# Performance work log

Measured on AMD Instinct MI355X. Metric: run time of the kernel, lower is better.

The kernel has to match this reference:

```python
import jax, jax.numpy as jnp
import numpy as np

D_MODEL = 1024
NUM_HEADS = 16
HEAD_DIM = D_MODEL // NUM_HEADS
ROPE_BASE = 10000.0


def _rotate_half(x):
    x1, x2 = jnp.split(x, 2, axis=-1)
    return jnp.concatenate([-x2, x1], axis=-1)


def _rope_cache(seq_len, head_dim, dtype):
    half = head_dim // 2
    inv_freq = 1.0 / (ROPE_BASE ** (jnp.arange(half, dtype=jnp.float32) / float(half)))
    t = jnp.arange(seq_len, dtype=jnp.float32)
    freqs = t[:, None] * inv_freq[None, :]          # [s, half]
    emb = jnp.concatenate([freqs, freqs], axis=-1)   # [s, head_dim]
    cos = jnp.cos(emb)[None, None, :, :].astype(dtype)  # [1,1,s,d]
    sin = jnp.sin(emb)[None, None, :, :].astype(dtype)
    return cos, sin


def setup_inputs() -> dict:
    key = jax.random.key(0)
    k1, k2, k3 = jax.random.split(key, 3)
    b, s = 4, 2048
    x = jax.random.normal(k1, (b, s, D_MODEL), dtype=jnp.float32)
    mask = jnp.ones((b, s), dtype=jnp.float32)
    Wqkv = jax.random.normal(k2, (D_MODEL, 3 * D_MODEL), dtype=jnp.float32) * (D_MODEL ** -0.5)
    Wout = jax.random.normal(k3, (D_MODEL, D_MODEL), dtype=jnp.float32) * (D_MODEL ** -0.5)
    return {"x": x, "mask": mask, "Wqkv": Wqkv, "Wout": Wout}


def reference(x, mask, Wqkv, Wout):
    b, s, _ = x.shape
    qkv = x @ Wqkv                                   # [b,s,3*d_model]
    q, k, v = jnp.split(qkv, 3, axis=-1)

    def split_heads(t):
        return t.reshape(b, s, NUM_HEADS, HEAD_DIM).transpose(0, 2, 1, 3)  # [b,h,s,d]

    q, k, v = map(split_heads, (q, k, v))
    cos, sin = _rope_cache(s, HEAD_DIM, x.dtype)
    q = q * cos + _rotate_half(q) * sin
    k = k * cos + _rotate_half(k) * sin

    scale = HEAD_DIM ** -0.5
    logits = jnp.einsum('bhid,bhjd->bhij', q, k) * scale
    logits = logits + (1.0 - mask)[:, None, None, :] * -1e9
    attn = jax.nn.softmax(logits, axis=-1)
    out = jnp.einsum('bhij,bhjd->bhid', attn, v)     # [b,h,s,d]
    out = out.transpose(0, 2, 1, 3).reshape(b, s, D_MODEL)
    return out @ Wout
```

## Files before the change

### kernel.cpp

```cpp
#include <hip/hip_runtime.h>

typedef unsigned short u16;
typedef unsigned int u32;
typedef int i32x2 __attribute__((ext_vector_type(2)));
typedef float f32x4 __attribute__((ext_vector_type(4)));
typedef float f32x16 __attribute__((ext_vector_type(16)));
typedef __bf16 bf16x8 __attribute__((ext_vector_type(8)));
typedef unsigned short u16x8 __attribute__((ext_vector_type(8)));
typedef unsigned short u16x4 __attribute__((ext_vector_type(4)));
typedef unsigned int u32x4 __attribute__((ext_vector_type(4)));

#define S_ 2048
#define DM 1024

#define LDS_U32(p) ((__attribute__((address_space(3))) unsigned int*)(p))
#define GLB_U32(p) ((const __attribute__((address_space(1))) unsigned int*)(p))

__device__ __forceinline__ u16 f2bf(float f) {
    unsigned int u = __float_as_uint(f);
    u += 0x7fffu + ((u >> 16) & 1u);
    return (u16)(u >> 16);
}
__device__ __forceinline__ float bf2f(u16 s) {
    return __uint_as_float(((unsigned int)s) << 16);
}
__device__ __forceinline__ float fast_exp2(float x) {
#if __has_builtin(__builtin_amdgcn_exp2f)
    return __builtin_amdgcn_exp2f(x);
#else
    return __expf(x * 0.69314718056f);
#endif
}

__global__ __launch_bounds__(256) void f32_to_bf16_kernel(const float* __restrict__ in,
                                                          u16* __restrict__ o, int n) {
    int i = (blockIdx.x * 256 + threadIdx.x) << 2;
    if (i >= n) return;
    float4 f = *(const float4*)&in[i];
    u16x4 r;
    r[0] = f2bf(f.x); r[1] = f2bf(f.y); r[2] = f2bf(f.z); r[3] = f2bf(f.w);
    *(u16x4*)&o[i] = r;
}

__global__ __launch_bounds__(256) void transpose_w(const float* __restrict__ W,
                                                   u16* __restrict__ Wt, int K, int N) {
    __shared__ float tile[32][33];
    int nb = blockIdx.x << 5, kb = blockIdx.y << 5;
    int tx = threadIdx.x & 31, ty = threadIdx.x >> 5;
#pragma unroll
    for (int r = 0; r < 32; r += 8)
        tile[ty + r][tx] = W[(size_t)(kb + ty + r) * N + nb + tx];
    __syncthreads();
#pragma unroll
    for (int r = 0; r < 32; r += 8)
        Wt[(size_t)(nb + ty + r) * K + kb + tx] = f2bf(tile[tx][ty + r]);
}

template <int MODE>
__global__ __launch_bounds__(256) void gemm_bt(const u16* __restrict__ A,
                                               const u16* __restrict__ Bt,
                                               float* __restrict__ Cf,
                                               u16* __restrict__ Qp, u16* __restrict__ Kp,
                                               u16* __restrict__ Vp,
                                               int M, int N, int K) {
    __shared__ __align__(16) u16 Al[128 * 32];
    __shared__ __align__(16) u16 Bl[128 * 32];
    const int tid = threadIdx.x;
    const int Ntiles = N >> 7;
    const int cpx = gridDim.x >> 3;
    const int bid = (int)blockIdx.x;
    const int wg = (bid & 7) * cpx + (bid >> 3);
    const int mt = wg / Ntiles, nt = wg % Ntiles;
    const int m0 = mt << 7, n0 = nt << 7;
    const int wave = tid >> 6, lane = tid & 63;
    const int wm = (wave >> 1) << 6, wn = (wave & 1) << 6;
    const int lr = lane & 15, lk = (lane >> 4) << 3;

    const int srow = (wave << 4) + (lane >> 2);
    const int scol = (lane & 3) << 3;

    f32x4 acc[4][4] = {};

    for (int k0 = 0; k0 < K; k0 += 32) {
        __syncthreads();
#pragma unroll
        for (int i = 0; i < 2; ++i) {
            const u16* ga = &A[(size_t)(m0 + srow + (i << 6)) * K + k0 + scol];
            const u16* gb = &Bt[(size_t)(n0 + srow + (i << 6)) * K + k0 + scol];
            __builtin_amdgcn_global_load_lds(GLB_U32(ga), LDS_U32(&Al[(wave << 9) + (i << 11)]), 16, 0, 0);
            __builtin_amdgcn_global_load_lds(GLB_U32(gb), LDS_U32(&Bl[(wave << 9) + (i << 11)]), 16, 0, 0);
        }
        __syncthreads();
        bf16x8 af[4], bfr[4];
#pragma unroll
        for (int i = 0; i < 4; ++i) {
            af[i]  = __builtin_bit_cast(bf16x8, *(const u16x8*)&Al[(wm + (i << 4) + lr) * 32 + lk]);
            bfr[i] = __builtin_bit_cast(bf16x8, *(const u16x8*)&Bl[(wn + (i << 4) + lr) * 32 + lk]);
        }
#pragma unroll
        for (int i = 0; i < 4; ++i)
#pragma unroll
            for (int j = 0; j < 4; ++j)
                acc[i][j] = __builtin_amdgcn_mfma_f32_16x16x32_bf16(af[i], bfr[j], acc[i][j], 0, 0, 0);
    }

    if (MODE == 0) {
        const int t = (n0 + wn) >> 10;
        if (t < 2) {
            const float LN1E4_32 = 9.210340371976184f / 32.0f;
            const float invf0 = __expf(-(float)lr * LN1E4_32);
            const float invf1 = __expf(-(float)(lr + 16) * LN1E4_32);
#pragma unroll
            for (int i = 0; i < 4; ++i) {
                const int rbase = m0 + wm + (i << 4) + ((lane >> 4) << 2);
#pragma unroll
                for (int jj = 0; jj < 4; ++jj) {
                    const float s = (float)((rbase + jj) & (S_ - 1));
                    float sn0, c0, sn1, c1;
                    __sincosf(s * invf0, &sn0, &c0);
                    __sincosf(s * invf1, &sn1, &c1);
                    const float v0 = acc[i][0][jj], v1 = acc[i][1][jj];
                    const float v2 = acc[i][2][jj], v3 = acc[i][3][jj];
                    acc[i][0][jj] = v0 * c0 - v2 * sn0;
                    acc[i][2][jj] = v2 * c0 + v0 * sn0;
                    acc[i][1][jj] = v1 * c1 - v3 * sn1;
                    acc[i][3][jj] = v3 * c1 + v1 * sn1;
                }
            }
        }
    }

#pragma unroll
    for (int i = 0; i < 4; ++i) {
#pragma unroll
        for (int j = 0; j < 4; ++j) {
            int rbase = m0 + wm + (i << 4) + ((lane >> 4) << 2);
            int col = n0 + wn + (j << 4) + lr;
#pragma unroll
            for (int jj = 0; jj < 4; ++jj) {
                float val = acc[i][j][jj];
                int row = rbase + jj;
                if (MODE == 0) {
                    int t = col >> 10, rem = col & 1023;
                    int h = rem >> 6, d = rem & 63;
                    int b = row >> 11, s = row & 2047;
                    size_t dst = ((size_t)((b << 4) + h) * S_ + s) * 64 + d;
                    u16 bv = f2bf(val);
                    if (t == 0) Qp[dst] = bv;
                    else if (t == 1) Kp[dst] = bv;
                    else Vp[dst] = bv;
                } else {
                    Cf[(size_t)row * N + col] = val;
                }
            }
        }
    }
}

__global__ __launch_bounds__(256) void vtrans_kernel(const u16* __restrict__ v,
                                                     u16* __restrict__ vt) {
    __shared__ __align__(16) u16 t[64][72];
    const int bh = blockIdx.x >> 5, st = blockIdx.x & 31;
    const size_t base = (size_t)bh * (S_ * 64);
    const int s0 = st << 6;
    const int r = threadIdx.x >> 2, c0 = (threadIdx.x & 3) << 4;
    *(u16x8*)&t[r][c0]     = *(const u16x8*)&v[base + (size_t)(s0 + r) * 64 + c0];
    *(u16x8*)&t[r][c0 + 8] = *(const u16x8*)&v[base + (size_t)(s0 + r) * 64 + c0 + 8];
    __syncthreads();
    u16x8 w0, w1;
#pragma unroll
    for (int i = 0; i < 8; ++i) w0[i] = t[c0 + i][r];
#pragma unroll
    for (int i = 0; i < 8; ++i) w1[i] = t[c0 + 8 + i][r];
    *(u16x8*)&vt[base + (size_t)r * S_ + s0 + c0]     = w0;
    *(u16x8*)&vt[base + (size_t)r * S_ + s0 + c0 + 8] = w1;
}

__device__ __forceinline__ void softmax_chain(f32x16* p, f32x16* acc,
                                              float& m_run, float& l_run,
                                              u32* wa, u32* wb,
                                              const float* madd_tile, bool hasmask,
                                              float* bcast_w, int c, int hi) {
    if (hasmask) {
#pragma unroll
        for (int tt = 0; tt < 2; ++tt)
#pragma unroll
            for (int rq = 0; rq < 4; ++rq) {
                float4 mf = *(const float4*)&madd_tile[tt * 32 + rq * 8 + hi * 4];
                p[tt][4 * rq + 0] += mf.x;
                p[tt][4 * rq + 1] += mf.y;
                p[tt][4 * rq + 2] += mf.z;
                p[tt][4 * rq + 3] += mf.w;
            }
    }

    float tm[16];
#pragma unroll
    for (int r = 0; r < 16; ++r) tm[r] = fmaxf(p[0][r], p[1][r]);
    float a0 = fmaxf(fmaxf(tm[0], tm[1]), tm[2]);
    float a1 = fmaxf(fmaxf(tm[3], tm[4]), tm[5]);
    float a2 = fmaxf(fmaxf(tm[6], tm[7]), tm[8]);
    float a3 = fmaxf(fmaxf(tm[9], tm[10]), tm[11]);
    float a4 = fmaxf(fmaxf(tm[12], tm[13]), tm[14]);
    float b0 = fmaxf(fmaxf(a0, a1), a2);
    float b1 = fmaxf(fmaxf(a3, a4), tm[15]);
    float mx = fmaxf(b0, b1);
    {
        i32x2 mm = __builtin_amdgcn_permlane32_swap(__float_as_int(mx), __float_as_int(mx), false, false);
        mx = fmaxf(__int_as_float(mm[0]), __int_as_float(mm[1]));
    }

    if (!__all(mx - m_run <= 8.0f)) {
        float mnew = fmaxf(m_run, mx);
        float alpha = fast_exp2(m_run - mnew);
        m_run = mnew;
        l_run *= alpha;
        bcast_w[c] = alpha;
        float avf[16];
#pragma unroll
        for (int rq = 0; rq < 4; ++rq) {
            float4 t4 = *(const float4*)&bcast_w[rq * 8 + hi * 4];
            avf[4 * rq + 0] = t4.x; avf[4 * rq + 1] = t4.y;
            avf[4 * rq + 2] = t4.z; avf[4 * rq + 3] = t4.w;
        }
#pragma unroll
        for (int r = 0; r < 16; ++r) {
            acc[0][r] *= avf[r];
            acc[1][r] *= avf[r];
        }
    }

    float s4[4] = {0.f, 0.f, 0.f, 0.f};
#pragma unroll
    for (int tt = 0; tt < 2; ++tt)
#pragma unroll
        for (int r = 0; r < 16; ++r) {
            float e = fast_exp2(p[tt][r] - m_run);
            p[tt][r] = e;
            s4[r & 3] += e;
        }
    float ls = (s4[0] + s4[1]) + (s4[2] + s4[3]);
    {
        i32x2 ss = __builtin_amdgcn_permlane32_swap(__float_as_int(ls), __float_as_int(ls), false, false);
        ls = __int_as_float(ss[0]) + __int_as_float(ss[1]);
    }
    l_run += ls;

#pragma unroll
    for (int tt = 0; tt < 2; ++tt)
#pragma unroll
        for (int rq = 0; rq < 4; ++rq) {
            float e0 = p[tt][4 * rq + 0], e1 = p[tt][4 * rq + 1];
            float e2 = p[tt][4 * rq + 2], e3 = p[tt][4 * rq + 3];
            u32 w0, w1;
            asm("v_cvt_pk_bf16_f32 %0, %1, %2" : "=v"(w0) : "v"(e0), "v"(e1));
            asm("v_cvt_pk_bf16_f32 %0, %1, %2" : "=v"(w1) : "v"(e2), "v"(e3));
            wa[4 * tt + rq] = w0;
            wb[4 * tt + rq] = w1;
        }
}

__global__ __launch_bounds__(256, 2) void attn_kernel(const u16* __restrict__ q,
                                                      const u16* __restrict__ k,
                                                      const u16* __restrict__ vt,
                                                      const float* __restrict__ mask,
                                                      u16* __restrict__ outp) {
    __shared__ __align__(16) u16 Kl[2][64 * 64];
    __shared__ __align__(16) u16 Vl[2][64 * 64];
    __shared__ float madd2[2][64];
    __shared__ float bcast[4][32];

    const int tid = threadIdx.x, wave = tid >> 6, lane = tid & 63;
    const int c = lane & 31, hi = lane >> 5, c7 = c & 7;
    const int bh = blockIdx.x & 63, qt = blockIdx.x >> 6;
    const int b = bh >> 4, h = bh & 15;
    const size_t base = (size_t)bh * (S_ * 64);
    const int qrowA = (qt << 8) + (wave << 5) + c;
    const int qrowB = qrowA + 128;

    const float QS = 0.18033688f;

    bf16x8 qfA[4], qfB[4];
#pragma unroll
    for (int j = 0; j < 4; ++j) {
        u16x8 rawA = *(const u16x8*)&q[base + (size_t)qrowA * 64 + j * 16 + hi * 8];
        u16x8 rawB = *(const u16x8*)&q[base + (size_t)qrowB * 64 + j * 16 + hi * 8];
        u16x8 scA, scB;
#pragma unroll
        for (int e = 0; e < 8; ++e) {
            scA[e] = f2bf(bf2f(rawA[e]) * QS);
            scB[e] = f2bf(bf2f(rawB[e]) * QS);
        }
        qfA[j] = __builtin_bit_cast(bf16x8, scA);
        qfB[j] = __builtin_bit_cast(bf16x8, scB);
    }

    f32x16 accA[2] = {}, accB[2] = {};
    float m_runA = -1e30f, l_runA = 0.f;
    float m_runB = -1e30f, l_runB = 0.f;

    const int sr = tid >> 2, su = (tid & 3) << 1;
    const int so0 = sr * 64 + ((su ^ (sr & 7)) << 3);
    const int so1 = sr * 64 + (((su + 1) ^ (sr & 7)) << 3);

    u16x8 kc0 = *(const u16x8*)&k[base + (size_t)sr * 64 + su * 8];
    u16x8 kc1 = *(const u16x8*)&k[base + (size_t)sr * 64 + su * 8 + 8];
    u16x8 vc0 = *(const u16x8*)&vt[base + (size_t)sr * S_ + su * 8];
    u16x8 vc1 = *(const u16x8*)&vt[base + (size_t)sr * S_ + su * 8 + 8];
    float mval = (tid < 64) ? mask[b * S_ + tid] : 1.0f;

    for (int t = 0; t < 32; ++t) {
        const int bi = t & 1;
        u16* Kb = &Kl[bi][0];
        u16* Vb = &Vl[bi][0];
        *(u16x8*)&Kb[so0] = kc0;
        *(u16x8*)&Kb[so1] = kc1;
        *(u16x8*)&Vb[so0] = vc0;
        *(u16x8*)&Vb[so1] = vc1;
        if (tid < 64) madd2[bi][tid] = (1.0f - mval) * -1.44269504e9f;
        if (t + 1 < 32) {
            const int kn = (t + 1) << 6;
            kc0 = *(const u16x8*)&k[base + (size_t)(kn + sr) * 64 + su * 8];
            kc1 = *(const u16x8*)&k[base + (size_t)(kn + sr) * 64 + su * 8 + 8];
            vc0 = *(const u16x8*)&vt[base + (size_t)sr * S_ + kn + su * 8];
            vc1 = *(const u16x8*)&vt[base + (size_t)sr * S_ + kn + su * 8 + 8];
            mval = (tid < 64) ? mask[b * S_ + kn + tid] : 1.0f;
        }
        __syncthreads();

        f32x16 pA[2] = {}, pB[2] = {};
        __builtin_amdgcn_s_setprio(1);
#pragma unroll
        for (int j = 0; j < 4; ++j) {
            const int uo = ((2 * j + hi) ^ c7) << 3;
            bf16x8 ka  = __builtin_bit_cast(bf16x8, *(const u16x8*)&Kb[c * 64 + uo]);
            bf16x8 kb2 = __builtin_bit_cast(bf16x8, *(const u16x8*)&Kb[(32 + c) * 64 + uo]);
            pA[0] = __builtin_amdgcn_mfma_f32_32x32x16_bf16(ka,  qfA[j], pA[0], 0, 0, 0);
            pA[1] = __builtin_amdgcn_mfma_f32_32x32x16_bf16(kb2, qfA[j], pA[1], 0, 0, 0);
            pB[0] = __builtin_amdgcn_mfma_f32_32x32x16_bf16(ka,  qfB[j], pB[0], 0, 0, 0);
            pB[1] = __builtin_amdgcn_mfma_f32_32x32x16_bf16(kb2, qfB[j], pB[1], 0, 0, 0);
        }
        __builtin_amdgcn_s_setprio(0);

        bool hasmask = __any(madd2[bi][lane] != 0.0f);

        u32 waA[8], wbA[8], waB[8], wbB[8];
        softmax_chain(pA, accA, m_runA, l_runA, waA, wbA, &madd2[bi][0], hasmask, &bcast[wave][0], c, hi);
        softmax_chain(pB, accB, m_runB, l_runB, waB, wbB, &madd2[bi][0], hasmask, &bcast[wave][0], c, hi);

        __builtin_amdgcn_s_setprio(1);
#pragma unroll
        for (int ks = 0; ks < 4; ++ks) {
            i32x2 raA = __builtin_amdgcn_permlane32_swap((int)waA[2 * ks], (int)waA[2 * ks + 1], false, false);
            i32x2 rbA = __builtin_amdgcn_permlane32_swap((int)wbA[2 * ks], (int)wbA[2 * ks + 1], false, false);
            i32x2 raB = __builtin_amdgcn_permlane32_swap((int)waB[2 * ks], (int)waB[2 * ks + 1], false, false);
            i32x2 rbB = __builtin_amdgcn_permlane32_swap((int)wbB[2 * ks], (int)wbB[2 * ks + 1], false, false);
            u32x4 pwA, pwB;
            pwA[0] = (u32)raA[0]; pwA[1] = (u32)rbA[0]; pwA[2] = (u32)raA[1]; pwA[3] = (u32)rbA[1];
            pwB[0] = (u32)raB[0]; pwB[1] = (u32)rbB[0]; pwB[2] = (u32)raB[1]; pwB[3] = (u32)rbB[1];
            bf16x8 pafA = __builtin_bit_cast(bf16x8, pwA);
            bf16x8 pafB = __builtin_bit_cast(bf16x8, pwB);
            const int uo = ((2 * ks + hi) ^ c7) << 3;
#pragma unroll
            for (int dt = 0; dt < 2; ++dt) {
                bf16x8 vf = __builtin_bit_cast(bf16x8,
                            *(const u16x8*)&Vb[(32 * dt + c) * 64 + uo]);
                accA[dt] = __builtin_amdgcn_mfma_f32_32x32x16_bf16(pafA, vf, accA[dt], 0, 0, 0);
                accB[dt] = __builtin_amdgcn_mfma_f32_32x32x16_bf16(pafB, vf, accB[dt], 0, 0, 0);
            }
        }
        __builtin_amdgcn_s_setprio(0);
    }

    {
        bcast[wave][c] = l_runA;
        __builtin_amdgcn_wave_barrier();
        float lvf[16];
#pragma unroll
        for (int rq = 0; rq < 4; ++rq) {
            float4 t4 = *(const float4*)&bcast[wave][rq * 8 + hi * 4];
            lvf[4 * rq + 0] = __builtin_amdgcn_rcpf(t4.x);
            lvf[4 * rq + 1] = __builtin_amdgcn_rcpf(t4.y);
            lvf[4 * rq + 2] = __builtin_amdgcn_rcpf(t4.z);
            lvf[4 * rq + 3] = __builtin_amdgcn_rcpf(t4.w);
        }
        const size_t orow0 = (size_t)b * S_ + (qt << 8) + (wave << 5);
#pragma unroll
        for (int dt = 0; dt < 2; ++dt)
#pragma unroll
            for (int r = 0; r < 16; ++r) {
                int qr = (r & 3) + 8 * (r >> 2) + 4 * hi;
                outp[(orow0 + qr) * DM + h * 64 + dt * 32 + c] = f2bf(accA[dt][r] * lvf[r]);
            }
    }
    {
        __builtin_amdgcn_wave_barrier();
        bcast[wave][c] = l_runB;
        __builtin_amdgcn_wave_barrier();
        float lvf[16];
#pragma unroll
        for (int rq = 0; rq < 4; ++rq) {
            float4 t4 = *(const float4*)&bcast[wave][rq * 8 + hi * 4];
            lvf[4 * rq + 0] = __builtin_amdgcn_rcpf(t4.x);
            lvf[4 * rq + 1] = __builtin_amdgcn_rcpf(t4.y);
            lvf[4 * rq + 2] = __builtin_amdgcn_rcpf(t4.z);
            lvf[4 * rq + 3] = __builtin_amdgcn_rcpf(t4.w);
        }
        const size_t orow0 = (size_t)b * S_ + (qt << 8) + (wave << 5) + 128;
#pragma unroll
        for (int dt = 0; dt < 2; ++dt)
#pragma unroll
            for (int r = 0; r < 16; ++r) {
                int qr = (r & 3) + 8 * (r >> 2) + 4 * hi;
                outp[(orow0 + qr) * DM + h * 64 + dt * 32 + c] = f2bf(accB[dt][r] * lvf[r]);
            }
    }
}

extern "C" void kernel_launch(void* const* d_in, const int* in_sizes, int n_in,
                              void* d_out, int out_size, void* d_ws, size_t ws_size,
                              hipStream_t stream) {
    const float* x    = (const float*)d_in[0];
    const float* mask = (const float*)d_in[1];
    const float* Wqkv = (const float*)d_in[2];
    const float* Wout = (const float*)d_in[3];
    float* out = (float*)d_out;
    char* ws = (char*)d_ws;
    const size_t MB = 1u << 20;
    u16* xb    = (u16*)(ws);
    u16* WqkvT = (u16*)(ws + 16 * MB);
    u16* WoutT = (u16*)(ws + 22 * MB);
    u16* qb    = (u16*)(ws + 24 * MB);
    u16* kb    = (u16*)(ws + 40 * MB);
    u16* vb    = (u16*)(ws + 56 * MB);
    u16* vtb   = xb;
    u16* ao    = vb;

    f32_to_bf16_kernel<<<8192, 256, 0, stream>>>(x, xb, 8192 * 1024);
    transpose_w<<<dim3(96, 32), 256, 0, stream>>>(Wqkv, WqkvT, 1024, 3072);
    transpose_w<<<dim3(32, 32), 256, 0, stream>>>(Wout, WoutT, 1024, 1024);
    gemm_bt<0><<<64 * 24, 256, 0, stream>>>(xb, WqkvT, nullptr, qb, kb, vb, 8192, 3072, 1024);
    vtrans_kernel<<<2048, 256, 0, stream>>>(vb, vtb);
    attn_kernel<<<512, 256, 0, stream>>>(qb, kb, vtb, mask, ao);
    gemm_bt<1><<<64 * 8, 256, 0, stream>>>(ao, WoutT, out, nullptr, nullptr, nullptr, 8192, 1024, 1024);
}
```

Baseline: 223.0 us.

## Write transposed V from QKV GEMM epilogue and compute softmax row sums via MFMA

The QKV GEMM epilogue now writes V directly in transposed [b,h,d,s] layout with packed 4-element stores, which removes the separate vtrans kernel and its extra read/write pass over V. Q/K stores are specialized per tile to avoid per-element branching. In attention, the softmax denominator is accumulated by an extra MFMA against a ones vector instead of per-lane exp sums plus a cross-lane swap, which also drops the LDS broadcast at the end. This trades a few extra matrix instructions per tile for less VALU and cross-lane work. The row sum is now built from the bf16-rounded probabilities, which changes rounding slightly.

```diff
diff --git a/kernel.cpp b/kernel.cpp
--- a/kernel.cpp
+++ b/kernel.cpp
@@ -61,7 +61,7 @@
                                                const u16* __restrict__ Bt,
                                                float* __restrict__ Cf,
                                                u16* __restrict__ Qp, u16* __restrict__ Kp,
-                                               u16* __restrict__ Vp,
+                                               u16* __restrict__ Vtp,
                                                int M, int N, int K) {
     __shared__ __align__(16) u16 Al[128 * 32];
     __shared__ __align__(16) u16 Bl[128 * 32];
@@ -127,58 +127,54 @@
                     acc[i][3][jj] = v3 * c1 + v1 * sn1;
                 }
             }
-        }
-    }
-
-#pragma unroll
-    for (int i = 0; i < 4; ++i) {
-#pragma unroll
-        for (int j = 0; j < 4; ++j) {
-            int rbase = m0 + wm + (i << 4) + ((lane >> 4) << 2);
-            int col = n0 + wn + (j << 4) + lr;
-#pragma unroll
-            for (int jj = 0; jj < 4; ++jj) {
-                float val = acc[i][j][jj];
-                int row = rbase + jj;
-                if (MODE == 0) {
-                    int t = col >> 10, rem = col & 1023;
-                    int h = rem >> 6, d = rem & 63;
-                    int b = row >> 11, s = row & 2047;
-                    size_t dst = ((size_t)((b << 4) + h) * S_ + s) * 64 + d;
-                    u16 bv = f2bf(val);
-                    if (t == 0) Qp[dst] = bv;
-                    else if (t == 1) Kp[dst] = bv;
-                    else Vp[dst] = bv;
-                } else {
-                    Cf[(size_t)row * N + col] = val;
+            u16* P = (t == 0) ? Qp : Kp;
+#pragma unroll
+            for (int i = 0; i < 4; ++i) {
+#pragma unroll
+                for (int j = 0; j < 4; ++j) {
+                    int rbase = m0 + wm + (i << 4) + ((lane >> 4) << 2);
+                    int col = n0 + wn + (j << 4) + lr;
+                    int h = (col & 1023) >> 6, d = col & 63;
+#pragma unroll
+                    for (int jj = 0; jj < 4; ++jj) {
+                        int row = rbase + jj;
+                        int b = row >> 11, s = row & 2047;
+                        P[((size_t)((b << 4) + h) * S_ + s) * 64 + d] = f2bf(acc[i][j][jj]);
+                    }
                 }
             }
-        }
-    }
-}
-
-__global__ __launch_bounds__(256) void vtrans_kernel(const u16* __restrict__ v,
-                                                     u16* __restrict__ vt) {
-    __shared__ __align__(16) u16 t[64][72];
-    const int bh = blockIdx.x >> 5, st = blockIdx.x & 31;
-    const size_t base = (size_t)bh * (S_ * 64);
-    const int s0 = st << 6;
-    const int r = threadIdx.x >> 2, c0 = (threadIdx.x & 3) << 4;
-    *(u16x8*)&t[r][c0]     = *(const u16x8*)&v[base + (size_t)(s0 + r) * 64 + c0];
-    *(u16x8*)&t[r][c0 + 8] = *(const u16x8*)&v[base + (size_t)(s0 + r) * 64 + c0 + 8];
-    __syncthreads();
-    u16x8 w0, w1;
-#pragma unroll
-    for (int i = 0; i < 8; ++i) w0[i] = t[c0 + i][r];
-#pragma unroll
-    for (int i = 0; i < 8; ++i) w1[i] = t[c0 + 8 + i][r];
-    *(u16x8*)&vt[base + (size_t)r * S_ + s0 + c0]     = w0;
-    *(u16x8*)&vt[base + (size_t)r * S_ + s0 + c0 + 8] = w1;
-}
-
-__device__ __forceinline__ void softmax_chain(f32x16* p, f32x16* acc,
-                                              float& m_run, float& l_run,
-                                              u32* wa, u32* wb,
+        } else {
+#pragma unroll
+            for (int i = 0; i < 4; ++i) {
+                const int rbase = m0 + wm + (i << 4) + ((lane >> 4) << 2);
+                const int b = rbase >> 11, sb = rbase & 2047;
+#pragma unroll
+                for (int j = 0; j < 4; ++j) {
+                    int col = n0 + wn + (j << 4) + lr;
+                    int h = (col & 1023) >> 6, d = col & 63;
+                    u16x4 pk;
+#pragma unroll
+                    for (int jj = 0; jj < 4; ++jj) pk[jj] = f2bf(acc[i][j][jj]);
+                    *(u16x4*)&Vtp[((size_t)((b << 4) + h) * 64 + d) * S_ + sb] = pk;
+                }
+            }
+        }
+    } else {
+#pragma unroll
+        for (int i = 0; i < 4; ++i)
+#pragma unroll
+            for (int j = 0; j < 4; ++j) {
+                int rbase = m0 + wm + (i << 4) + ((lane >> 4) << 2);
+                int col = n0 + wn + (j << 4) + lr;
+#pragma unroll
+                for (int jj = 0; jj < 4; ++jj)
+                    Cf[(size_t)(rbase + jj) * N + col] = acc[i][j][jj];
+            }
+    }
+}
+
+__device__ __forceinline__ void softmax_chain(f32x16* p, f32x16* acc, f32x16& accS,
+                                              float& m_run, u32* wa, u32* wb,
                                               const float* madd_tile, bool hasmask,
                                               float* bcast_w, int c, int hi) {
     if (hasmask) {
@@ -214,7 +210,6 @@
         float mnew = fmaxf(m_run, mx);
         float alpha = fast_exp2(m_run - mnew);
         m_run = mnew;
-        l_run *= alpha;
         bcast_w[c] = alpha;
         float avf[16];
 #pragma unroll
@@ -227,24 +222,15 @@
         for (int r = 0; r < 16; ++r) {
             acc[0][r] *= avf[r];
             acc[1][r] *= avf[r];
-        }
-    }
-
-    float s4[4] = {0.f, 0.f, 0.f, 0.f};
+            accS[r]   *= avf[r];
+        }
+    }
+
 #pragma unroll
     for (int tt = 0; tt < 2; ++tt)
 #pragma unroll
-        for (int r = 0; r < 16; ++r) {
-            float e = fast_exp2(p[tt][r] - m_run);
-            p[tt][r] = e;
-            s4[r & 3] += e;
-        }
-    float ls = (s4[0] + s4[1]) + (s4[2] + s4[3]);
-    {
-        i32x2 ss = __builtin_amdgcn_permlane32_swap(__float_as_int(ls), __float_as_int(ls), false, false);
-        ls = __int_as_float(ss[0]) + __int_as_float(ss[1]);
-    }
-    l_run += ls;
+        for (int r = 0; r < 16; ++r)
+            p[tt][r] = fast_exp2(p[tt][r] - m_run);
 
 #pragma unroll
     for (int tt = 0; tt < 2; ++tt)
@@ -295,9 +281,14 @@
         qfB[j] = __builtin_bit_cast(bf16x8, scB);
     }
 
+    u16x8 ou;
+#pragma unroll
+    for (int e = 0; e < 8; ++e) ou[e] = 0x3F80;
+    const bf16x8 onesf = __builtin_bit_cast(bf16x8, ou);
+
     f32x16 accA[2] = {}, accB[2] = {};
-    float m_runA = -1e30f, l_runA = 0.f;
-    float m_runB = -1e30f, l_runB = 0.f;
+    f32x16 accSA = {}, accSB = {};
+    float m_runA = -1e30f, m_runB = -1e30f;
 
     const int sr = tid >> 2, su = (tid & 3) << 1;
     const int so0 = sr * 64 + ((su ^ (sr & 7)) << 3);
@@ -345,8 +336,8 @@
         bool hasmask = __any(madd2[bi][lane] != 0.0f);
 
         u32 waA[8], wbA[8], waB[8], wbB[8];
-        softmax_chain(pA, accA, m_runA, l_runA, waA, wbA, &madd2[bi][0], hasmask, &bcast[wave][0], c, hi);
-        softmax_chain(pB, accB, m_runB, l_runB, waB, wbB, &madd2[bi][0], hasmask, &bcast[wave][0], c, hi);
+        softmax_chain(pA, accA, accSA, m_runA, waA, wbA, &madd2[bi][0], hasmask, &bcast[wave][0], c, hi);
+        softmax_chain(pB, accB, accSB, m_runB, waB, wbB, &madd2[bi][0], hasmask, &bcast[wave][0], c, hi);
 
         __builtin_amdgcn_s_setprio(1);
 #pragma unroll
@@ -360,6 +351,8 @@
             pwB[0] = (u32)raB[0]; pwB[1] = (u32)rbB[0]; pwB[2] = (u32)raB[1]; pwB[3] = (u32)rbB[1];
             bf16x8 pafA = __builtin_bit_cast(bf16x8, pwA);
             bf16x8 pafB = __builtin_bit_cast(bf16x8, pwB);
+            accSA = __builtin_amdgcn_mfma_f32_32x32x16_bf16(pafA, onesf, accSA, 0, 0, 0);
+            accSB = __builtin_amdgcn_mfma_f32_32x32x16_bf16(pafB, onesf, accSB, 0, 0, 0);
             const int uo = ((2 * ks + hi) ^ c7) << 3;
 #pragma unroll
             for (int dt = 0; dt < 2; ++dt) {
@@ -373,46 +366,25 @@
     }
 
     {
-        bcast[wave][c] = l_runA;
-        __builtin_amdgcn_wave_barrier();
-        float lvf[16];
-#pragma unroll
-        for (int rq = 0; rq < 4; ++rq) {
-            float4 t4 = *(const float4*)&bcast[wave][rq * 8 + hi * 4];
-            lvf[4 * rq + 0] = __builtin_amdgcn_rcpf(t4.x);
-            lvf[4 * rq + 1] = __builtin_amdgcn_rcpf(t4.y);
-            lvf[4 * rq + 2] = __builtin_amdgcn_rcpf(t4.z);
-            lvf[4 * rq + 3] = __builtin_amdgcn_rcpf(t4.w);
-        }
         const size_t orow0 = (size_t)b * S_ + (qt << 8) + (wave << 5);
 #pragma unroll
         for (int dt = 0; dt < 2; ++dt)
 #pragma unroll
             for (int r = 0; r < 16; ++r) {
                 int qr = (r & 3) + 8 * (r >> 2) + 4 * hi;
-                outp[(orow0 + qr) * DM + h * 64 + dt * 32 + c] = f2bf(accA[dt][r] * lvf[r]);
+                outp[(orow0 + qr) * DM + h * 64 + dt * 32 + c] =
+                    f2bf(accA[dt][r] * __builtin_amdgcn_rcpf(accSA[r]));
             }
     }
     {
-        __builtin_amdgcn_wave_barrier();
-        bcast[wave][c] = l_runB;
-        __builtin_amdgcn_wave_barrier();
-        float lvf[16];
-#pragma unroll
-        for (int rq = 0; rq < 4; ++rq) {
-            float4 t4 = *(const float4*)&bcast[wave][rq * 8 + hi * 4];
-            lvf[4 * rq + 0] = __builtin_amdgcn_rcpf(t4.x);
-            lvf[4 * rq + 1] = __builtin_amdgcn_rcpf(t4.y);
-            lvf[4 * rq + 2] = __builtin_amdgcn_rcpf(t4.z);
-            lvf[4 * rq + 3] = __builtin_amdgcn_rcpf(t4.w);
-        }
         const size_t orow0 = (size_t)b * S_ + (qt << 8) + (wave << 5) + 128;
 #pragma unroll
         for (int dt = 0; dt < 2; ++dt)
 #pragma unroll
             for (int r = 0; r < 16; ++r) {
                 int qr = (r & 3) + 8 * (r >> 2) + 4 * hi;
-                outp[(orow0 + qr) * DM + h * 64 + dt * 32 + c] = f2bf(accB[dt][r] * lvf[r]);
+                outp[(orow0 + qr) * DM + h * 64 + dt * 32 + c] =
+                    f2bf(accB[dt][r] * __builtin_amdgcn_rcpf(accSB[r]));
             }
     }
 }
@@ -432,15 +404,13 @@
     u16* WoutT = (u16*)(ws + 22 * MB);
     u16* qb    = (u16*)(ws + 24 * MB);
     u16* kb    = (u16*)(ws + 40 * MB);
-    u16* vb    = (u16*)(ws + 56 * MB);
-    u16* vtb   = xb;
-    u16* ao    = vb;
+    u16* vtb   = (u16*)(ws + 56 * MB);
+    u16* ao    = xb;
 
     f32_to_bf16_kernel<<<8192, 256, 0, stream>>>(x, xb, 8192 * 1024);
     transpose_w<<<dim3(96, 32), 256, 0, stream>>>(Wqkv, WqkvT, 1024, 3072);
     transpose_w<<<dim3(32, 32), 256, 0, stream>>>(Wout, WoutT, 1024, 1024);
-    gemm_bt<0><<<64 * 24, 256, 0, stream>>>(xb, WqkvT, nullptr, qb, kb, vb, 8192, 3072, 1024);
-    vtrans_kernel<<<2048, 256, 0, stream>>>(vb, vtb);
+    gemm_bt<0><<<64 * 24, 256, 0, stream>>>(xb, WqkvT, nullptr, qb, kb, vtb, 8192, 3072, 1024);
     attn_kernel<<<512, 256, 0, stream>>>(qb, kb, vtb, mask, ao);
     gemm_bt<1><<<64 * 8, 256, 0, stream>>>(ao, WoutT, out, nullptr, nullptr, nullptr, 8192, 1024, 1024);
 }
```

Result: faster. 218.5 us (-2.0%).
